# Kernel optimization log

Hardware: AMD Instinct MI355X
Metric: run time of the kernel (lower is better)

The kernel has to match this reference:

```python
import jax, jax.numpy as jnp
import numpy as np
from jax import lax

BN_EPS = 1e-5


def conv3x3(x, w):
    # x: [B,C,H,W], w: [O,I,3,3] -> [B,O,H,W], stride 1, SAME padding, no bias
    return lax.conv_general_dilated(x, w, (1, 1), 'SAME',
                                    dimension_numbers=('NCHW', 'OIHW', 'NCHW'))


def batchnorm_eval(x, gamma, beta, mean, var):
    inv = gamma / jnp.sqrt(var + BN_EPS)
    return x * inv[None, :, None, None] + (beta - mean * inv)[None, :, None, None]


def avg_pool3(x):
    # AvgPool2d(3, stride=1, padding=1) with count_include_pad=True -> sum/9
    s = lax.reduce_window(x, 0.0, lax.add, (1, 1, 3, 3), (1, 1, 1, 1), 'SAME')
    return s / 9.0


def max_pool3(x):
    return lax.reduce_window(x, -jnp.inf, lax.max, (1, 1, 3, 3), (1, 1, 1, 1), 'SAME')


def setup_inputs() -> dict:
    key = jax.random.key(0)
    ks = jax.random.split(key, 20)
    B, C, H, W = 8, 256, 48, 48
    sc = 0.05
    inp = {
        'ftr': jax.random.normal(ks[0], (B, C, H, W), jnp.float32),
        'wq': jax.random.normal(ks[1], (C, C, 1, 1), jnp.float32) * sc,
        'bq': jax.random.normal(ks[2], (C,), jnp.float32) * sc,
        'wk': jax.random.normal(ks[3], (C, C, 1, 1), jnp.float32) * sc,
        'bk': jax.random.normal(ks[4], (C,), jnp.float32) * sc,
        'wv': jax.random.normal(ks[5], (C, C, 1, 1), jnp.float32) * sc,
        'bv': jax.random.normal(ks[6], (C,), jnp.float32) * sc,
        'delta': jnp.array([0.1], jnp.float32),
        'w_rbc': jax.random.normal(ks[7], (C, C, 3, 3), jnp.float32) * sc,
        'g1': jnp.ones((C,), jnp.float32),
        'b1': jnp.zeros((C,), jnp.float32),
        'm1': jnp.zeros((C,), jnp.float32),
        'v1': jnp.ones((C,), jnp.float32),
        'w_rbc2': jax.random.normal(ks[8], (C, 2 * C, 3, 3), jnp.float32) * sc,
        'g2': jnp.ones((C,), jnp.float32),
        'b2': jnp.zeros((C,), jnp.float32),
        'm2': jnp.zeros((C,), jnp.float32),
        'v2': jnp.ones((C,), jnp.float32),
    }
    return inp


def reference(ftr, wq, bq, wk, bk, wv, bv, delta, w_rbc, g1, b1, m1, v1,
              w_rbc2, g2, b2, m2, v2):
    B, C, H, W = ftr.shape
    P = H * W
    x = ftr.reshape(B, C, P)  # [B,C,P]
    # 1x1 convs as channel matmuls
    q = jnp.einsum('oc,bcp->bop', wq[:, :, 0, 0], x) + bq[None, :, None]
    k = jnp.einsum('oc,bcp->bop', wk[:, :, 0, 0], x) + bk[None, :, None]
    v = jnp.einsum('oc,bcp->bop', wv[:, :, 0, 0], x) + bv[None, :, None]
    # scores[b,i,j] = sum_c q[b,c,i] * k[b,c,j]; softmax over i (dim=1)
    scores = jnp.einsum('bci,bcj->bij', q, k)
    weights = jax.nn.softmax(scores, axis=1)
    G = jnp.einsum('bci,bij->bcj', v, weights).reshape(B, C, H, W)
    out = delta[0] * G + ftr
    # conv_rbc: conv3x3 -> BN(eval) -> ReLU, then sigmoid gate
    out = jax.nn.relu(batchnorm_eval(conv3x3(out, w_rbc), g1, b1, m1, v1))
    gate = jax.nn.sigmoid(out)
    ftr_avg = avg_pool3(ftr) * gate
    ftr_max = max_pool3(ftr) * gate
    cat = jnp.concatenate((ftr_max, ftr_avg), axis=1)  # [B,2C,H,W]
    out = jax.nn.relu(batchnorm_eval(conv3x3(cat, w_rbc2), g2, b2, m2, v2))
    return out
```

## Files before the change

### kernel.cpp

```cpp
#include <hip/hip_runtime.h>
#include <math.h>

#define NB   8
#define CCH  256
#define PPX  2304
#define CPb  (CCH*PPX)
#define NTOT (NB*CPb)
#define PSQ  (PPX*PPX)
#define PADIMG 2500

typedef short short8_t __attribute__((ext_vector_type(8)));
typedef float f4_t __attribute__((ext_vector_type(4)));

__device__ __forceinline__ float relu_(float x){ return x > 0.f ? x : 0.f; }

__device__ __forceinline__ unsigned short f2bf(float f) {
  unsigned int u = __builtin_bit_cast(unsigned int, f);
  u += 0x7fffu + ((u >> 16) & 1u);
  return (unsigned short)(u >> 16);
}
__device__ __forceinline__ float bf2f(unsigned short h) {
  unsigned int u = ((unsigned int)h) << 16;
  return __builtin_bit_cast(float, u);
}
__device__ __forceinline__ unsigned int pack2(float a, float b) {
  return (unsigned int)f2bf(a) | ((unsigned int)f2bf(b) << 16);
}

__device__ __forceinline__ void gll16(const void* g, void* l) {
  __builtin_amdgcn_global_load_lds(
      (const __attribute__((address_space(1))) unsigned int*)g,
      (__attribute__((address_space(3))) unsigned int*)l, 16, 0, 0);
}

__global__ __launch_bounds__(256) void castw(
    const float* __restrict__ w, unsigned short* __restrict__ o, int n)
{
  const int i = blockIdx.x * 256 + threadIdx.x;
  if (i < n) o[i] = f2bf(w[i]);
}

__global__ __launch_bounds__(256) void repack_w(
    const float* __restrict__ w, unsigned short* __restrict__ wr, int Cin)
{
  const int idx = blockIdx.x * 256 + threadIdx.x;
  const int total = 9 * 256 * Cin;
  if (idx >= total) return;
  const int c = idx % Cin;
  const int rest = idx / Cin;
  const int o = rest % 256;
  const int tap = rest / 256;
  wr[idx] = f2bf(w[((size_t)o * Cin + c) * 9 + tap]);
}

__global__ __launch_bounds__(256) void transpose_cast(
    const float* __restrict__ ftr, unsigned short* __restrict__ xt)
{
  const int p0 = blockIdx.x * 64, c0 = blockIdx.y * 64, b = blockIdx.z;
  const int t = threadIdx.x;
  __shared__ unsigned short T[64][72];
  #pragma unroll
  for (int pass = 0; pass < 4; pass++) {
    const int cr = pass * 16 + (t >> 4);
    const int pc = (t & 15) * 4;
    float4 v = *(const float4*)&ftr[((size_t)(b * 256 + c0 + cr)) * PPX + p0 + pc];
    T[pc + 0][cr] = f2bf(v.x); T[pc + 1][cr] = f2bf(v.y);
    T[pc + 2][cr] = f2bf(v.z); T[pc + 3][cr] = f2bf(v.w);
  }
  __syncthreads();
  #pragma unroll
  for (int pass = 0; pass < 2; pass++) {
    const int pr = pass * 32 + (t >> 3);
    const int cc = (t & 7) * 8;
    *(uint4*)&xt[((size_t)(b * PPX + p0 + pr)) * 256 + c0 + cc] = *(const uint4*)&T[pr][cc];
  }
}

template<int EPI>
__global__ __launch_bounds__(256) void gemm_nt(
    const unsigned short* __restrict__ A, long Ab,
    const unsigned short* __restrict__ B, long Bb, int K,
    unsigned short* __restrict__ O, long Ob, int ldo,
    const float* __restrict__ bias,
    const float* __restrict__ ftr, const float* __restrict__ delta, int bstart)
{
  const int t = threadIdx.x;
  const int ln = t & 63;
  const int wid = t >> 6;
  const int wm = (wid & 1) * 64, wn = (wid >> 1) * 64;
  const int lm = ln & 15, lg = ln >> 4;
  const int m0 = blockIdx.x * 128, n0 = blockIdx.y * 128;
  const long bz = blockIdx.z;
  const unsigned short* Ap = A + bz * Ab;
  const unsigned short* Bp = B + bz * Bb;

  __shared__ __align__(16) unsigned short As[128 * 32];
  __shared__ __align__(16) unsigned short Bs[128 * 32];

  const int sR = ln >> 2, sP = ln & 3;
  const int fbase = lm * 32 + (((lg + (lm >> 2)) & 3) * 8);

  f4_t acc[4][4];
  #pragma unroll
  for (int i = 0; i < 4; i++)
    #pragma unroll
    for (int j = 0; j < 4; j++) acc[i][j] = (f4_t){0.f, 0.f, 0.f, 0.f};

  for (int k0 = 0; k0 < K; k0 += 32) {
    __syncthreads();
    #pragma unroll
    for (int i = wid; i < 8; i += 4) {
      const int R = i * 16 + sR;
      const int l = (sP - (R >> 2)) & 3;
      gll16(Ap + (size_t)(m0 + R) * K + k0 + l * 8, As + i * 512);
      gll16(Bp + (size_t)(n0 + R) * K + k0 + l * 8, Bs + i * 512);
    }
    __syncthreads();
    short8_t a[4], b[4];
    #pragma unroll
    for (int ti = 0; ti < 4; ti++)
      a[ti] = *(const short8_t*)(As + (wm + ti * 16) * 32 + fbase);
    #pragma unroll
    for (int tj = 0; tj < 4; tj++)
      b[tj] = *(const short8_t*)(Bs + (wn + tj * 16) * 32 + fbase);
    #pragma unroll
    for (int ti = 0; ti < 4; ti++)
      #pragma unroll
      for (int tj = 0; tj < 4; tj++)
        acc[ti][tj] = __builtin_amdgcn_mfma_f32_16x16x32_bf16(
            a[ti], b[tj], acc[ti][tj], 0, 0, 0);
  }

  if (EPI == 3) {
    const int b = bstart + (int)bz;
    const float d0 = delta[0];
    #pragma unroll
    for (int ti = 0; ti < 4; ti++) {
      const int mb = m0 + wm + ti * 16 + (lg << 2);
      #pragma unroll
      for (int tj = 0; tj < 4; tj++) {
        const int n = n0 + wn + tj * 16 + lm;
        const int y = n / 48, x = n - (n / 48) * 48;
        const size_t pp = (size_t)(y + 1) * 50 + (x + 1);
        float vr[4];
        #pragma unroll
        for (int r = 0; r < 4; r++)
          vr[r] = d0 * acc[ti][tj][r] + ftr[((size_t)(b * 256 + mb + r)) * PPX + n];
        uint2 o;
        o.x = pack2(vr[0], vr[1]);
        o.y = pack2(vr[2], vr[3]);
        *(uint2*)(O + ((size_t)b * PADIMG + pp) * 256 + mb) = o;
      }
    }
  } else {
    #pragma unroll
    for (int ti = 0; ti < 4; ti++) {
      const int mb = m0 + wm + ti * 16 + (lg << 2);
      #pragma unroll
      for (int tj = 0; tj < 4; tj++) {
        const int n = n0 + wn + tj * 16 + lm;
        float add0 = 0.f, add1 = 0.f, add2 = 0.f, add3 = 0.f;
        if (EPI == 1) { add0 = bias[mb]; add1 = bias[mb+1]; add2 = bias[mb+2]; add3 = bias[mb+3]; }
        if (EPI == 2) { add0 = add1 = add2 = add3 = bias[n]; }
        uint2 o;
        o.x = pack2(acc[ti][tj][0] + add0, acc[ti][tj][1] + add1);
        o.y = pack2(acc[ti][tj][2] + add2, acc[ti][tj][3] + add3);
        *(uint2*)(O + bz * Ob + (size_t)n * ldo + mb) = o;
      }
    }
  }
}

__global__ __launch_bounds__(256) void rowstats(
    unsigned short* __restrict__ St, long sstride)
{
  const int j = blockIdx.x, bb = blockIdx.y;
  unsigned short* row = St + (long)bb * sstride + (size_t)j * PPX;
  const int t = threadIdx.x;

  float v[16];
  int nv = 0;
  float m = -1e30f;
  for (int ch = t; ch < 288; ch += 256) {
    const uint4 d = *(const uint4*)(row + ch * 8);
    const unsigned int* dp = (const unsigned int*)&d;
    #pragma unroll
    for (int q = 0; q < 4; q++) {
      v[nv]     = bf2f((unsigned short)(dp[q] & 0xffffu));
      v[nv + 1] = bf2f((unsigned short)(dp[q] >> 16));
      m = fmaxf(m, fmaxf(v[nv], v[nv + 1]));
      nv += 2;
    }
  }
  __shared__ float red[256];
  red[t] = m; __syncthreads();
  for (int s = 128; s > 0; s >>= 1) {
    if (t < s) red[t] = fmaxf(red[t], red[t + s]);
    __syncthreads();
  }
  m = red[0]; __syncthreads();
  float sum = 0.f;
  for (int u = 0; u < nv; u++) { v[u] = expf(v[u] - m); sum += v[u]; }
  red[t] = sum; __syncthreads();
  for (int s = 128; s > 0; s >>= 1) {
    if (t < s) red[t] += red[t + s];
    __syncthreads();
  }
  const float inv = 1.f / red[0];
  int u = 0;
  for (int ch = t; ch < 288; ch += 256) {
    unsigned int res[4];
    #pragma unroll
    for (int q = 0; q < 4; q++) {
      res[q] = pack2(v[u] * inv, v[u + 1] * inv);
      u += 2;
    }
    *(uint4*)(row + ch * 8) = *(const uint4*)res;
  }
}

template<bool OUT_BF16>
__global__ __launch_bounds__(128) void conv_mfma(
    const unsigned short* __restrict__ act_p, int Cin,
    const unsigned short* __restrict__ wr,
    const float* __restrict__ gamma, const float* __restrict__ beta,
    const float* __restrict__ mean,  const float* __restrict__ var,
    void* __restrict__ outv)
{
  const int t  = threadIdx.x;
  const int wv = t >> 6;
  const int ln = t & 63;
  const int lm = ln & 15;
  const int lg = ln >> 4;

  const int bx = blockIdx.x;
  const int bb = bx / 18;
  const int p0 = (bx % 18) * 128;
  const int m0 = blockIdx.y * 64;

  __shared__ __align__(16) unsigned short Bs[240 * 32];
  __shared__ __align__(16) unsigned short As[9 * 64 * 32];

  const int qbase = p0 + 2 * (p0 / 48);
  int qoff[4];
  #pragma unroll
  for (int tj = 0; tj < 4; tj++) {
    const int p = p0 + wv * 64 + tj * 16 + lm;
    qoff[tj] = (p - p0) + 2 * (p / 48 - p0 / 48) + 51;
  }

  const int sR = ln >> 2, sP = ln & 3;
  const int abase = lm * 32 + (((lg + (lm >> 2)) & 3) * 8);

  f4_t acc[4][4];
  #pragma unroll
  for (int i = 0; i < 4; i++)
    #pragma unroll
    for (int j = 0; j < 4; j++) acc[i][j] = (f4_t){0.f, 0.f, 0.f, 0.f};

  for (int c0 = 0; c0 < Cin; c0 += 32) {
    __syncthreads();
    const unsigned short* gb = act_p + ((size_t)bb * PADIMG) * Cin + c0;
    for (int i = wv; i < 15; i += 2) {
      const int R = i * 16 + sR;
      int Rg = qbase + R;
      if (Rg > PADIMG - 1) Rg = PADIMG - 1;
      const int l = (sP - (R >> 2)) & 3;
      gll16(gb + (size_t)Rg * Cin + l * 8, Bs + i * 512);
    }
    for (int i = wv; i < 36; i += 2) {
      const int R = i * 16 + sR;
      const int tap = R >> 6, mr = R & 63;
      const int l = (sP - (R >> 2)) & 3;
      gll16(wr + ((size_t)(tap * 256 + m0 + mr)) * Cin + c0 + l * 8, As + i * 512);
    }
    __syncthreads();
    #pragma unroll
    for (int ky = 0; ky < 3; ky++) {
      #pragma unroll
      for (int kx = 0; kx < 3; kx++) {
        const int off = (ky - 1) * 50 + (kx - 1);
        const int tap = ky * 3 + kx;
        short8_t a[4], b[4];
        #pragma unroll
        for (int ti = 0; ti < 4; ti++)
          a[ti] = *(const short8_t*)(As + tap * 2048 + ti * 512 + abase);
        #pragma unroll
        for (int tj = 0; tj < 4; tj++) {
          const int R = qoff[tj] + off;
          const int slot = (lg + (R >> 2)) & 3;
          b[tj] = *(const short8_t*)(Bs + R * 32 + slot * 8);
        }
        #pragma unroll
        for (int ti = 0; ti < 4; ti++)
          #pragma unroll
          for (int tj = 0; tj < 4; tj++)
            acc[ti][tj] = __builtin_amdgcn_mfma_f32_16x16x32_bf16(
                a[ti], b[tj], acc[ti][tj], 0, 0, 0);
      }
    }
  }

  #pragma unroll
  for (int ti = 0; ti < 4; ti++) {
    const int m = m0 + ti * 16 + (lg << 2);
    float inv[4], add[4];
    #pragma unroll
    for (int r = 0; r < 4; r++) {
      inv[r] = gamma[m + r] * rsqrtf(var[m + r] + 1e-5f);
      add[r] = beta[m + r] - mean[m + r] * inv[r];
    }
    #pragma unroll
    for (int tj = 0; tj < 4; tj++) {
      const int p = p0 + wv * 64 + tj * 16 + lm;
      float vr[4];
      #pragma unroll
      for (int r = 0; r < 4; r++)
        vr[r] = relu_(acc[ti][tj][r] * inv[r] + add[r]);
      if (OUT_BF16) {
        uint2 o;
        o.x = pack2(vr[0], vr[1]);
        o.y = pack2(vr[2], vr[3]);
        *(uint2*)((unsigned short*)outv + ((size_t)(bb * PPX + p)) * 256 + m) = o;
      } else {
        #pragma unroll
        for (int r = 0; r < 4; r++)
          ((float*)outv)[((size_t)(bb * 256 + m + r)) * PPX + p] = vr[r];
      }
    }
  }
}

__global__ __launch_bounds__(256) void pool_gate_cat(
    const unsigned short* __restrict__ xt, const unsigned short* __restrict__ act1b,
    unsigned short* __restrict__ cat_p)
{
  const int idx = blockIdx.x * 256 + threadIdx.x;
  const int c = idx & 255;
  const int rest = idx >> 8;
  const int p = rest % PPX;
  const int b = rest / PPX;
  const int y = p / 48, x = p - (p / 48) * 48;
  const unsigned short* base = xt + ((size_t)b * PPX) * 256 + c;
  float s = 0.f, mxv = -1e30f;
  #pragma unroll
  for (int dy = -1; dy <= 1; dy++) {
    const int yy = y + dy;
    if (yy < 0 || yy >= 48) continue;
    #pragma unroll
    for (int dx = -1; dx <= 1; dx++) {
      const int xx = x + dx;
      if (xx < 0 || xx >= 48) continue;
      const float f = bf2f(base[(size_t)(yy * 48 + xx) * 256]);
      s += f; mxv = fmaxf(mxv, f);
    }
  }
  const float g = bf2f(act1b[(size_t)idx]);
  const float gate = 1.f / (1.f + expf(-g));
  const size_t pp = (size_t)(y + 1) * 50 + (x + 1);
  unsigned short* crow = cat_p + ((size_t)b * PADIMG + pp) * 512;
  crow[c]       = f2bf(mxv * gate);
  crow[c + 256] = f2bf(s * (1.f / 9.f) * gate);
}

extern "C" void kernel_launch(void* const* d_in, const int* in_sizes, int n_in,
                              void* d_out, int out_size, void* d_ws, size_t ws_size,
                              hipStream_t stream)
{
  const float* ftr  = (const float*)d_in[0];
  const float* wq   = (const float*)d_in[1];
  const float* bq   = (const float*)d_in[2];
  const float* wk   = (const float*)d_in[3];
  const float* bk   = (const float*)d_in[4];
  const float* wv   = (const float*)d_in[5];
  const float* bv   = (const float*)d_in[6];
  const float* delta= (const float*)d_in[7];
  const float* w1   = (const float*)d_in[8];
  const float* g1   = (const float*)d_in[9];
  const float* b1   = (const float*)d_in[10];
  const float* m1   = (const float*)d_in[11];
  const float* v1   = (const float*)d_in[12];
  const float* w2   = (const float*)d_in[13];
  const float* g2   = (const float*)d_in[14];
  const float* b2   = (const float*)d_in[15];
  const float* m2   = (const float*)d_in[16];
  const float* v2   = (const float*)d_in[17];
  float* out = (float*)d_out;

  const size_t XT = (size_t)NTOT;
  unsigned short* base = (unsigned short*)d_ws;
  unsigned short* xt   = base;
  unsigned short* qt   = xt  + XT;
  unsigned short* kt   = qt  + XT;
  unsigned short* vbuf = kt  + XT;
  unsigned short* wqb  = vbuf + XT;
  unsigned short* wkb  = wqb + 65536;
  unsigned short* wvb  = wkb + 65536;
  unsigned short* wr1  = wvb + 65536;
  unsigned short* wr2  = wr1 + (size_t)9 * 256 * 256;
  unsigned short* attn_p = wr2 + (size_t)9 * 256 * 512;
  unsigned short* act1b  = attn_p + (size_t)NB * PADIMG * 256;
  unsigned short* cat_p  = act1b + XT;
  unsigned short* St     = cat_p + (size_t)NB * PADIMG * 512;

  const size_t head_bytes = (size_t)((char*)St - (char*)base);
  const bool modeA = ws_size >= head_bytes + (size_t)NB * PSQ * 2;

  const size_t ATTN_P_SH = (size_t)NB * PADIMG * 256;
  const size_t CAT_P_SH  = (size_t)NB * PADIMG * 512;

  castw<<<dim3(256), 256, 0, stream>>>(wq, wqb, 65536);
  castw<<<dim3(256), 256, 0, stream>>>(wk, wkb, 65536);
  castw<<<dim3(256), 256, 0, stream>>>(wv, wvb, 65536);
  repack_w<<<dim3((9 * 256 * 256 + 255) / 256), 256, 0, stream>>>(w1, wr1, 256);
  repack_w<<<dim3((9 * 256 * 512 + 255) / 256), 256, 0, stream>>>(w2, wr2, 512);

  transpose_cast<<<dim3(36, 4, 8), 256, 0, stream>>>(ftr, xt);

  gemm_nt<1><<<dim3(2, 18, 8), 256, 0, stream>>>(
      wqb, 0L, xt, (long)CPb, 256, qt, (long)CPb, 256, bq, nullptr, nullptr, 0);
  gemm_nt<1><<<dim3(2, 18, 8), 256, 0, stream>>>(
      wkb, 0L, xt, (long)CPb, 256, kt, (long)CPb, 256, bk, nullptr, nullptr, 0);
  gemm_nt<2><<<dim3(18, 2, 8), 256, 0, stream>>>(
      xt, (long)CPb, wvb, 0L, 256, vbuf, (long)CPb, PPX, bv, nullptr, nullptr, 0);

  hipMemsetAsync(attn_p, 0, ATTN_P_SH * 2, stream);

  if (modeA) {
    gemm_nt<0><<<dim3(18, 18, 8), 256, 0, stream>>>(
        qt, (long)CPb, kt, (long)CPb, 256, St, (long)PSQ, PPX, nullptr, nullptr, nullptr, 0);
    rowstats<<<dim3(PPX, 8), 256, 0, stream>>>(St, (long)PSQ);
    gemm_nt<3><<<dim3(2, 18, 8), 256, 0, stream>>>(
        vbuf, (long)CPb, St, (long)PSQ, PPX, attn_p, 0L, 0, nullptr, ftr, delta, 0);
  } else {
    for (int b = 0; b < NB; b++) {
      gemm_nt<0><<<dim3(18, 18, 1), 256, 0, stream>>>(
          qt + (size_t)b * CPb, 0L, kt + (size_t)b * CPb, 0L, 256,
          St, 0L, PPX, nullptr, nullptr, nullptr, 0);
      rowstats<<<dim3(PPX, 1), 256, 0, stream>>>(St, 0L);
      gemm_nt<3><<<dim3(2, 18, 1), 256, 0, stream>>>(
          vbuf + (size_t)b * CPb, 0L, St, 0L, PPX, attn_p, 0L, 0, nullptr, ftr, delta, b);
    }
  }

  conv_mfma<true><<<dim3(144, 4), 128, 0, stream>>>(
      attn_p, 256, wr1, g1, b1, m1, v1, (void*)act1b);

  hipMemsetAsync(cat_p, 0, CAT_P_SH * 2, stream);
  pool_gate_cat<<<dim3(NTOT / 256), 256, 0, stream>>>(xt, act1b, cat_p);

  conv_mfma<false><<<dim3(144, 4), 128, 0, stream>>>(
      cat_p, 512, wr2, g2, b2, m2, v2, (void*)out);
}
```

Baseline: 453.7 us.

## Split conv K across two blocks, double-buffer GEMM LDS, zero only pad borders

The 3x3 convolutions are split over two halves of the input channels via a grid z dimension, doubling block count from 576 to 1152 to better fill the GPU. Partial sums go to an fp32 workspace, and separate combine kernels apply BN, ReLU and the output layout. The GEMM kernel gains double-buffered LDS so the next K slice loads while the current one is computed. The full memsets of the padded buffers become a small kernel that zeroes only the border pixels. In exchange, the split adds extra fp32 partial traffic and two more launches.

```diff
diff --git a/kernel.cpp b/kernel.cpp
--- a/kernel.cpp
+++ b/kernel.cpp
@@ -51,6 +51,23 @@
   const int o = rest % 256;
   const int tap = rest / 256;
   wr[idx] = f2bf(w[((size_t)o * Cin + c) * 9 + tap]);
+}
+
+__global__ __launch_bounds__(64) void zero_borders(
+    unsigned short* __restrict__ img, int C)
+{
+  const int b = blockIdx.x / 196;
+  const int e = blockIdx.x % 196;
+  int pos;
+  if (e < 50)       pos = e;
+  else if (e < 100) pos = 2450 + (e - 50);
+  else if (e < 148) pos = (e - 99) * 50;
+  else              pos = (e - 147) * 50 + 49;
+  const int c = threadIdx.x * 8;
+  if (c < C) {
+    uint4 z = {0u, 0u, 0u, 0u};
+    *(uint4*)(img + ((size_t)b * PADIMG + pos) * C + c) = z;
+  }
 }
 
 __global__ __launch_bounds__(256) void transpose_cast(
@@ -94,8 +111,8 @@
   const unsigned short* Ap = A + bz * Ab;
   const unsigned short* Bp = B + bz * Bb;
 
-  __shared__ __align__(16) unsigned short As[128 * 32];
-  __shared__ __align__(16) unsigned short Bs[128 * 32];
+  __shared__ __align__(16) unsigned short As[2][128 * 32];
+  __shared__ __align__(16) unsigned short Bs[2][128 * 32];
 
   const int sR = ln >> 2, sP = ln & 3;
   const int fbase = lm * 32 + (((lg + (lm >> 2)) & 3) * 8);
@@ -106,23 +123,37 @@
     #pragma unroll
     for (int j = 0; j < 4; j++) acc[i][j] = (f4_t){0.f, 0.f, 0.f, 0.f};
 
-  for (int k0 = 0; k0 < K; k0 += 32) {
+  const int S = K / 32;
+
+  #pragma unroll
+  for (int i = wid; i < 8; i += 4) {
+    const int R = i * 16 + sR;
+    const int l = (sP - (R >> 2)) & 3;
+    gll16(Ap + (size_t)(m0 + R) * K + l * 8, &As[0][i * 512]);
+    gll16(Bp + (size_t)(n0 + R) * K + l * 8, &Bs[0][i * 512]);
+  }
+
+  for (int s = 0; s < S; s++) {
     __syncthreads();
-    #pragma unroll
-    for (int i = wid; i < 8; i += 4) {
-      const int R = i * 16 + sR;
-      const int l = (sP - (R >> 2)) & 3;
-      gll16(Ap + (size_t)(m0 + R) * K + k0 + l * 8, As + i * 512);
-      gll16(Bp + (size_t)(n0 + R) * K + k0 + l * 8, Bs + i * 512);
-    }
-    __syncthreads();
+    if (s + 1 < S) {
+      const int kk = (s + 1) * 32;
+      #pragma unroll
+      for (int i = wid; i < 8; i += 4) {
+        const int R = i * 16 + sR;
+        const int l = (sP - (R >> 2)) & 3;
+        gll16(Ap + (size_t)(m0 + R) * K + kk + l * 8, &As[(s + 1) & 1][i * 512]);
+        gll16(Bp + (size_t)(n0 + R) * K + kk + l * 8, &Bs[(s + 1) & 1][i * 512]);
+      }
+    }
+    const unsigned short* Asb = As[s & 1];
+    const unsigned short* Bsb = Bs[s & 1];
     short8_t a[4], b[4];
     #pragma unroll
     for (int ti = 0; ti < 4; ti++)
-      a[ti] = *(const short8_t*)(As + (wm + ti * 16) * 32 + fbase);
+      a[ti] = *(const short8_t*)(Asb + (wm + ti * 16) * 32 + fbase);
     #pragma unroll
     for (int tj = 0; tj < 4; tj++)
-      b[tj] = *(const short8_t*)(Bs + (wn + tj * 16) * 32 + fbase);
+      b[tj] = *(const short8_t*)(Bsb + (wn + tj * 16) * 32 + fbase);
     #pragma unroll
     for (int ti = 0; ti < 4; ti++)
       #pragma unroll
@@ -219,13 +250,10 @@
   }
 }
 
-template<bool OUT_BF16>
-__global__ __launch_bounds__(128) void conv_mfma(
+__global__ __launch_bounds__(128) void conv_part(
     const unsigned short* __restrict__ act_p, int Cin,
     const unsigned short* __restrict__ wr,
-    const float* __restrict__ gamma, const float* __restrict__ beta,
-    const float* __restrict__ mean,  const float* __restrict__ var,
-    void* __restrict__ outv)
+    float* __restrict__ part)
 {
   const int t  = threadIdx.x;
   const int wv = t >> 6;
@@ -237,6 +265,8 @@
   const int bb = bx / 18;
   const int p0 = (bx % 18) * 128;
   const int m0 = blockIdx.y * 64;
+  const int zz = blockIdx.z;
+  const int c_start = zz * (Cin >> 1);
 
   __shared__ __align__(16) unsigned short Bs[240 * 32];
   __shared__ __align__(16) unsigned short As[9 * 64 * 32];
@@ -258,7 +288,8 @@
     #pragma unroll
     for (int j = 0; j < 4; j++) acc[i][j] = (f4_t){0.f, 0.f, 0.f, 0.f};
 
-  for (int c0 = 0; c0 < Cin; c0 += 32) {
+  const int cend = c_start + (Cin >> 1);
+  for (int c0 = c_start; c0 < cend; c0 += 32) {
     __syncthreads();
     const unsigned short* gb = act_p + ((size_t)bb * PADIMG) * Cin + c0;
     for (int i = wv; i < 15; i += 2) {
@@ -301,33 +332,65 @@
     }
   }
 
+  float* pb = part + (size_t)zz * NB * PPX * 256;
   #pragma unroll
   for (int ti = 0; ti < 4; ti++) {
     const int m = m0 + ti * 16 + (lg << 2);
-    float inv[4], add[4];
-    #pragma unroll
-    for (int r = 0; r < 4; r++) {
-      inv[r] = gamma[m + r] * rsqrtf(var[m + r] + 1e-5f);
-      add[r] = beta[m + r] - mean[m + r] * inv[r];
-    }
     #pragma unroll
     for (int tj = 0; tj < 4; tj++) {
       const int p = p0 + wv * 64 + tj * 16 + lm;
-      float vr[4];
-      #pragma unroll
-      for (int r = 0; r < 4; r++)
-        vr[r] = relu_(acc[ti][tj][r] * inv[r] + add[r]);
-      if (OUT_BF16) {
-        uint2 o;
-        o.x = pack2(vr[0], vr[1]);
-        o.y = pack2(vr[2], vr[3]);
-        *(uint2*)((unsigned short*)outv + ((size_t)(bb * PPX + p)) * 256 + m) = o;
-      } else {
-        #pragma unroll
-        for (int r = 0; r < 4; r++)
-          ((float*)outv)[((size_t)(bb * 256 + m + r)) * PPX + p] = vr[r];
-      }
-    }
+      *(f4_t*)(pb + ((size_t)(bb * PPX + p)) * 256 + m) = acc[ti][tj];
+    }
+  }
+}
+
+__global__ __launch_bounds__(256) void combine_pc(
+    const float* __restrict__ part,
+    const float* __restrict__ gamma, const float* __restrict__ beta,
+    const float* __restrict__ mean,  const float* __restrict__ var,
+    unsigned short* __restrict__ outb)
+{
+  const size_t idx = (size_t)blockIdx.x * 256 + threadIdx.x;
+  const int c = (int)(idx & 255);
+  const float v = part[idx] + part[(size_t)NB * PPX * 256 + idx];
+  const float inv = gamma[c] * rsqrtf(var[c] + 1e-5f);
+  const float add = beta[c] - mean[c] * inv;
+  outb[idx] = f2bf(relu_(v * inv + add));
+}
+
+__global__ __launch_bounds__(256) void combine_cp(
+    const float* __restrict__ part,
+    const float* __restrict__ gamma, const float* __restrict__ beta,
+    const float* __restrict__ mean,  const float* __restrict__ var,
+    float* __restrict__ out)
+{
+  const int p0 = blockIdx.x * 64, c0 = blockIdx.y * 64, b = blockIdx.z;
+  const int t = threadIdx.x;
+  __shared__ float T[64][68];
+  const size_t poff = (size_t)NB * PPX * 256;
+  #pragma unroll
+  for (int pass = 0; pass < 4; pass++) {
+    const int pr = pass * 16 + (t >> 4);
+    const int cc = (t & 15) * 4;
+    const size_t row = ((size_t)(b * PPX + p0 + pr)) * 256 + c0 + cc;
+    const float4 v0 = *(const float4*)(part + row);
+    const float4 v1 = *(const float4*)(part + poff + row);
+    const float vs[4] = {v0.x + v1.x, v0.y + v1.y, v0.z + v1.z, v0.w + v1.w};
+    #pragma unroll
+    for (int i = 0; i < 4; i++) {
+      const int c = c0 + cc + i;
+      const float inv = gamma[c] * rsqrtf(var[c] + 1e-5f);
+      const float add = beta[c] - mean[c] * inv;
+      T[cc + i][pr] = relu_(vs[i] * inv + add);
+    }
+  }
+  __syncthreads();
+  #pragma unroll
+  for (int pass = 0; pass < 4; pass++) {
+    const int cr = pass * 16 + (t >> 4);
+    const int pc = (t & 15) * 4;
+    *(float4*)&out[((size_t)(b * 256 + c0 + cr)) * PPX + p0 + pc] =
+        *(const float4*)&T[cr][pc];
   }
 }
 
@@ -401,19 +464,20 @@
   unsigned short* attn_p = wr2 + (size_t)9 * 256 * 512;
   unsigned short* act1b  = attn_p + (size_t)NB * PADIMG * 256;
   unsigned short* cat_p  = act1b + XT;
-  unsigned short* St     = cat_p + (size_t)NB * PADIMG * 512;
+  float* part = (float*)(cat_p + (size_t)NB * PADIMG * 512);
+  unsigned short* St     = (unsigned short*)(part + (size_t)2 * NB * PPX * 256);
 
   const size_t head_bytes = (size_t)((char*)St - (char*)base);
   const bool modeA = ws_size >= head_bytes + (size_t)NB * PSQ * 2;
-
-  const size_t ATTN_P_SH = (size_t)NB * PADIMG * 256;
-  const size_t CAT_P_SH  = (size_t)NB * PADIMG * 512;
 
   castw<<<dim3(256), 256, 0, stream>>>(wq, wqb, 65536);
   castw<<<dim3(256), 256, 0, stream>>>(wk, wkb, 65536);
   castw<<<dim3(256), 256, 0, stream>>>(wv, wvb, 65536);
   repack_w<<<dim3((9 * 256 * 256 + 255) / 256), 256, 0, stream>>>(w1, wr1, 256);
   repack_w<<<dim3((9 * 256 * 512 + 255) / 256), 256, 0, stream>>>(w2, wr2, 512);
+
+  zero_borders<<<dim3(NB * 196), 64, 0, stream>>>(attn_p, 256);
+  zero_borders<<<dim3(NB * 196), 64, 0, stream>>>(cat_p, 512);
 
   transpose_cast<<<dim3(36, 4, 8), 256, 0, stream>>>(ftr, xt);
 
@@ -423,8 +487,6 @@
       wkb, 0L, xt, (long)CPb, 256, kt, (long)CPb, 256, bk, nullptr, nullptr, 0);
   gemm_nt<2><<<dim3(18, 2, 8), 256, 0, stream>>>(
       xt, (long)CPb, wvb, 0L, 256, vbuf, (long)CPb, PPX, bv, nullptr, nullptr, 0);
-
-  hipMemsetAsync(attn_p, 0, ATTN_P_SH * 2, stream);
 
   if (modeA) {
     gemm_nt<0><<<dim3(18, 18, 8), 256, 0, stream>>>(
@@ -443,12 +505,11 @@
     }
   }
 
-  conv_mfma<true><<<dim3(144, 4), 128, 0, stream>>>(
-      attn_p, 256, wr1, g1, b1, m1, v1, (void*)act1b);
-
-  hipMemsetAsync(cat_p, 0, CAT_P_SH * 2, stream);
+  conv_part<<<dim3(144, 4, 2), 128, 0, stream>>>(attn_p, 256, wr1, part);
+  combine_pc<<<dim3(NTOT / 256), 256, 0, stream>>>(part, g1, b1, m1, v1, act1b);
+
   pool_gate_cat<<<dim3(NTOT / 256), 256, 0, stream>>>(xt, act1b, cat_p);
 
-  conv_mfma<false><<<dim3(144, 4), 128, 0, stream>>>(
-      cat_p, 512, wr2, g2, b2, m2, v2, (void*)out);
-}
+  conv_part<<<dim3(144, 4, 2), 128, 0, stream>>>(cat_p, 512, wr2, part);
+  combine_cp<<<dim3(36, 4, 8), 256, 0, stream>>>(part, g2, b2, m2, v2, out);
+}
```

After: 474.9 us. 1.05x slower.
